# Optimization experiments

Measured on AMD Instinct MI355X. Metric: run time of the kernel, lower is better.

Reference implementation:

```python
import jax, jax.numpy as jnp
import numpy as np

B, T, P = 256, 1024, 32
HOME = 0  # home_idx from init_kwargs


def setup_inputs() -> dict:
    key = jax.random.key(0)
    k1, k2 = jax.random.split(key, 2)
    U = jax.random.normal(k1, (B, T, P), dtype=jnp.float32)
    A = jax.random.uniform(k2, (P, P), dtype=jnp.float32, minval=-0.01, maxval=0.01)
    bias = jnp.zeros((P,), dtype=jnp.float32)
    return {"unary_logits_btp": U, "A": A, "bias": bias}


def reference(unary_logits_btp, A, bias):
    """Constrained Viterbi decode (enforce at least one non-home state).
    State is (purpose p, visited-nonhome flag v in {0,1}). Returns paths (B,T) int32."""
    U = unary_logits_btp + bias  # (B,T,P), bias broadcast as in decode()
    Bn, Tn, Pn = U.shape
    NEG = jnp.finfo(U.dtype).min / 4
    is_home = jnp.arange(Pn) == HOME  # (P,)

    # t=0: v=0 only at home, v=1 only at non-home
    d0 = jnp.where(is_home, U[:, 0], NEG)
    d1 = jnp.where(is_home, NEG, U[:, 0])
    delta0 = jnp.stack([d0, d1], axis=-1)  # (B,P,2)

    def step(delta, U_t):
        # prev{v}[b, q, p] = delta[b, q, v] + A[q, p]
        prev0 = delta[:, :, 0][:, :, None] + A  # (B,P,P)
        prev1 = delta[:, :, 1][:, :, None] + A
        a0 = jnp.argmax(prev0, axis=1).astype(jnp.int32)
        v0 = jnp.max(prev0, axis=1)  # (B,P)
        a1 = jnp.argmax(prev1, axis=1).astype(jnp.int32)
        v1 = jnp.max(prev1, axis=1)
        use1 = v1 > v0  # strict >, matching torch.where(val_from1 > val_from0, ...)
        bval = jnp.where(use1, v1, v0)
        bq = jnp.where(use1, a1, a0)
        bv = use1.astype(jnp.int32)
        # next v=0 reachable only at home (from prev v=0)
        dn0 = jnp.where(is_home, v0 + U_t, NEG)
        # next v=1: home from prev v=1; non-home from best of prev v=0/v=1
        dn1 = jnp.where(is_home, v1, bval) + U_t
        p1 = jnp.where(is_home, a1, bq)
        vv1 = jnp.where(is_home, 1, bv).astype(jnp.int32)
        delta_new = jnp.stack([dn0, dn1], axis=-1)          # (B,P,2)
        psi_p = jnp.stack([a0, p1], axis=-1)                # (B,P,2) best prev purpose
        psi_v = jnp.stack([jnp.zeros_like(vv1), vv1], -1)   # (B,P,2) best prev flag
        return delta_new, (psi_p, psi_v)

    Us = jnp.swapaxes(U, 0, 1)  # (T,B,P)
    delta_T, (psi_p, psi_v) = jax.lax.scan(step, delta0, Us[1:])  # psi_*: (T-1,B,P,2)

    last_p = jnp.argmax(delta_T[:, :, 1], axis=1).astype(jnp.int32)  # (B,)
    b_idx = jnp.arange(Bn)

    def back(carry, psi):
        y, v = carry  # (B,), (B,)
        pp, pv = psi  # (B,P,2)
        py = pp[b_idx, y, v]
        nv = pv[b_idx, y, v]
        return (py, nv), py

    _, ys = jax.lax.scan(back, (last_p, jnp.ones((Bn,), jnp.int32)), (psi_p, psi_v),
                         reverse=True)  # ys: (T-1,B) with ys[t] = y[t]
    paths = jnp.concatenate([jnp.swapaxes(ys, 0, 1), last_p[:, None]], axis=1)  # (B,T)
    return paths
```

## Files before the change

### kernel.cpp

```cpp
#include <hip/hip_runtime.h>

#define T_LEN 1024
#define P_DIM 32
#define HOME_IDX 0
#define NCHUNK 32
#define CHUNK 32


__launch_bounds__(1024, 1)
__global__ void crf_viterbi_kernel(const float* __restrict__ U,
                                   const float* __restrict__ A,
                                   const float* __restrict__ bias,
                                   int* __restrict__ out)
{
    __shared__ __align__(16) float sdelta[P_DIM];
    __shared__ unsigned char spsi[(T_LEN - 1) * P_DIM];
    __shared__ unsigned char Mmap[NCHUNK * P_DIM];
    __shared__ unsigned char ent[NCHUNK];
    __shared__ int last_p_sh;

    const int tid = threadIdx.x;
    const int b   = blockIdx.x;
    int* __restrict__ outb = out + (size_t)b * T_LEN;

    if (tid < 64) {
        const int lane = tid;
        const int p    = lane & 31;
        const int h    = lane >> 5;
        const float NEG = -(3.4028234663852886e38f / 4.0f);

        float Areg[16];
#pragma unroll
        for (int j = 0; j < 16; ++j)
            Areg[j] = A[(16 * h + j) * P_DIM + p];
        const float A0p    = A[p];
        const float A00    = A[0];
        const float bias_p = bias[p];
        const float bias0  = bias[0];
        const int   q0     = h << 4;
        const bool  is_home = (p == HOME_IDX);

        const float4* __restrict__ sd4 = (const float4*)sdelta;
        const float* __restrict__ Ub = U + (size_t)b * T_LEN * P_DIM;

        const float u00 = Ub[p] + bias_p;
        float delta1  = is_home ? NEG : u00;
        float delta0h = Ub[HOME_IDX] + bias0;

        float L0 = Ub[1 * P_DIM + p];
        float L1 = Ub[2 * P_DIM + p];
        float L2 = Ub[3 * P_DIM + p];
        float L3 = Ub[4 * P_DIM + p];

        float Ut_n = L0 + bias_p;
        float u0_n = __shfl(Ut_n, 0);

        sdelta[p] = delta1;
        float4 R0 = sd4[4 * h + 0];
        float4 R1 = sd4[4 * h + 1];
        float4 R2 = sd4[4 * h + 2];
        float4 R3 = sd4[4 * h + 3];

        float cA[16], cB[16];
        float bvp = 0.f, ovvp = 0.f, bv2 = 0.f, ovv2 = 0.f;
        bool  condp = false, cond2 = false;
        int   ia2 = 0, io2 = 0;

#define STEP(t, F1, F2, CC, CP, Lc, Lr) do {                                   \
    const float Ut  = Ut_n;                                                    \
    const float u0c = u0_n;                                                    \
    CC[0]  = R0.x + Areg[0];  CC[1]  = R0.y + Areg[1];                         \
    CC[2]  = R0.z + Areg[2];  CC[3]  = R0.w + Areg[3];                         \
    CC[4]  = R1.x + Areg[4];  CC[5]  = R1.y + Areg[5];                         \
    CC[6]  = R1.z + Areg[6];  CC[7]  = R1.w + Areg[7];                         \
    CC[8]  = R2.x + Areg[8];  CC[9]  = R2.y + Areg[9];                         \
    CC[10] = R2.z + Areg[10]; CC[11] = R2.w + Areg[11];                        \
    CC[12] = R3.x + Areg[12]; CC[13] = R3.y + Areg[13];                        \
    CC[14] = R3.z + Areg[14]; CC[15] = R3.w + Areg[15];                        \
    const float g0 = fmaxf(fmaxf(CC[0],  CC[1]),  CC[2]);                      \
    const float g1 = fmaxf(fmaxf(CC[3],  CC[4]),  CC[5]);                      \
    const float g2 = fmaxf(fmaxf(CC[6],  CC[7]),  CC[8]);                      \
    const float g3 = fmaxf(fmaxf(CC[9],  CC[10]), CC[11]);                     \
    const float g4 = fmaxf(fmaxf(CC[12], CC[13]), CC[14]);                     \
    const float h0 = fmaxf(fmaxf(g0, g1), g2);                                 \
    const float h1 = fmaxf(fmaxf(g3, g4), CC[15]);                             \
    const float bv = fmaxf(h0, h1);                                            \
            \
    const float ovv = __shfl_xor(bv, 32);                                      \
    int ia1 = 0, io1 = 0;                                                      \
    if (F1) {        \
        ia1 = q0 + 15;                                                         \
        _Pragma("unroll")                                                      \
        for (int j = 14; j >= 0; --j)                                          \
            if (CP[j] == bvp) ia1 = q0 + j;                                    \
        io1 = __shfl_xor(ia1, 32);                                             \
    }                                                                          \
    if (F2) {      \
        const int amin = (ia2 < io2) ? ia2 : io2;                              \
        int a1 = (bv2 > ovv2) ? ia2 : io2;                                     \
        a1 = (bv2 == ovv2) ? amin : a1;                                        \
        spsi[(size_t)((t) - 3) * P_DIM + p] =                                  \
            (unsigned char)(cond2 ? (a1 | 32) : 0);                            \
    }                                                                          \
    const float v1 = fmaxf(bv, ovv);              \
    const float v0 = delta0h + A0p;                                            \
    const bool  use1 = (v1 > v0);                    \
    const bool  cond = use1 || is_home;                                        \
    const float sel  = cond ? v1 : v0;                                         \
    const float dn1  = sel + Ut;                                               \
    delta0h = (delta0h + A00) + u0c;                                           \
        \
    sdelta[p] = dn1;                                                           \
    R0 = sd4[4 * h + 0];                                                       \
    R1 = sd4[4 * h + 1];                                                       \
    R2 = sd4[4 * h + 2];                                                       \
    R3 = sd4[4 * h + 3];                                                       \
                                 \
    Ut_n = (Lc) + bias_p;                                                      \
    u0_n = __shfl(Ut_n, 0);                                                    \
    { int tn = (t) + 4; if (tn > T_LEN - 1) tn = T_LEN - 1;                    \
      (Lr) = Ub[(size_t)tn * P_DIM + p]; }                                     \
                                                          \
    bv2 = bvp; ovv2 = ovvp; cond2 = condp;                                     \
    ia2 = ia1; io2 = io1;                                                      \
    bvp = bv; ovvp = ovv; condp = cond;                                        \
    delta1 = dn1;                                                              \
} while (0)

        STEP(1, 0, 0, cA, cB, L1, L0);
        STEP(2, 1, 0, cB, cA, L2, L1);
        STEP(3, 1, 1, cA, cB, L3, L2);
        for (int t = 4; t <= T_LEN - 4; t += 4) {
            STEP(t + 0, 1, 1, cB, cA, L0, L3);
            STEP(t + 1, 1, 1, cA, cB, L1, L0);
            STEP(t + 2, 1, 1, cB, cA, L2, L1);
            STEP(t + 3, 1, 1, cA, cB, L3, L2);
        }
#undef STEP

        {
            const int amin = (ia2 < io2) ? ia2 : io2;
            int a1 = (bv2 > ovv2) ? ia2 : io2;
            a1 = (bv2 == ovv2) ? amin : a1;
            spsi[(size_t)(T_LEN - 3) * P_DIM + p] =
                (unsigned char)(cond2 ? (a1 | 32) : 0);
        }
        {
            int ia = q0 + 15;
#pragma unroll
            for (int j = 14; j >= 0; --j)
                if (cA[j] == bvp) ia = q0 + j;
            const int oia  = __shfl_xor(ia, 32);
            const int amin = (ia < oia) ? ia : oia;
            int a1 = (bvp > ovvp) ? ia : oia;
            a1 = (bvp == ovvp) ? amin : a1;
            spsi[(size_t)(T_LEN - 2) * P_DIM + p] =
                (unsigned char)(condp ? (a1 | 32) : 0);
        }

        float mv = delta1;
        int   mi = p;
#pragma unroll
        for (int m = 16; m >= 1; m >>= 1) {
            float ov = __shfl_xor(mv, m);
            int   oi = __shfl_xor(mi, m);
            bool take = (ov > mv) || ((ov == mv) && (oi < mi));
            mv = take ? ov : mv;
            mi = take ? oi : mi;
        }
        if (lane == 0) {
            outb[T_LEN - 1] = mi;
            last_p_sh = mi;
        }
    }

    __syncthreads();

    {
        const int c  = tid >> 5;
        const int pp = tid & 31;
        const int i_hi = min((c + 1) * CHUNK, T_LEN - 1);
        const int i_lo = c * CHUNK;
        int y = pp, v = 1;
        for (int i = i_hi - 1; i >= i_lo; --i) {
            const int bt = spsi[i * P_DIM + y];
            const int py = v ? (bt & 31) : 0;
            const int nv = v ? ((bt >> 5) & 1) : 0;
            y = py; v = nv;
        }
        Mmap[c * P_DIM + pp] = (unsigned char)(y | (v << 5));
    }
    __syncthreads();

    if (tid == 0) {
        int y = last_p_sh, v = 1;
        for (int c = NCHUNK - 1; c >= 0; --c) {
            ent[c] = (unsigned char)(y | (v << 5));
            if (v) {
                const int m = Mmap[c * P_DIM + y];
                y = m & 31;
                v = (m >> 5) & 1;
            } else {
                y = 0; v = 0;
            }
        }
    }
    __syncthreads();

    if (tid < NCHUNK) {
        const int c = tid;
        const int i_hi = min((c + 1) * CHUNK, T_LEN - 1);
        const int i_lo = c * CHUNK;
        const int e = ent[c];
        int y = e & 31;
        int v = (e >> 5) & 1;
        for (int i = i_hi - 1; i >= i_lo; --i) {
            const int bt = spsi[i * P_DIM + y];
            const int py = v ? (bt & 31) : 0;
            const int nv = v ? ((bt >> 5) & 1) : 0;
            outb[i] = py;
            y = py; v = nv;
        }
    }
}

extern "C" void kernel_launch(void* const* d_in, const int* in_sizes, int n_in,
                              void* d_out, int out_size, void* d_ws, size_t ws_size,
                              hipStream_t stream) {
    const float* U    = (const float*)d_in[0];
    const float* A    = (const float*)d_in[1];
    const float* bias = (const float*)d_in[2];
    int* out = (int*)d_out;

    const int B = in_sizes[0] / (T_LEN * P_DIM);
    crf_viterbi_kernel<<<B, 1024, 0, stream>>>(U, A, bias, out);
}
```

Before: 304.5 us.

## Remove cross-half shuffle from Viterbi critical path via split partial-max buffer

Each half-wave now writes its own partial max, combined with the v0 candidate and the unary term, into a double-width shared buffer. Every lane reads both halves' 16 entries and folds them with fmax during the next step's candidate computation. This takes the cross-half __shfl_xor and the v1/v0 select out of the serial recurrence. The use1/cond decisions needed for backpointers are recomputed later, off the critical path. In exchange each step does twice the LDS reads and extra fmax operations, and needs more registers.

```diff
diff --git a/kernel.cpp b/kernel.cpp
--- a/kernel.cpp
+++ b/kernel.cpp
@@ -13,7 +13,7 @@
                                    const float* __restrict__ bias,
                                    int* __restrict__ out)
 {
-    __shared__ __align__(16) float sdelta[P_DIM];
+    __shared__ __align__(16) float sw[2 * P_DIM];
     __shared__ unsigned char spsi[(T_LEN - 1) * P_DIM];
     __shared__ unsigned char Mmap[NCHUNK * P_DIM];
     __shared__ unsigned char ent[NCHUNK];
@@ -40,11 +40,11 @@
         const int   q0     = h << 4;
         const bool  is_home = (p == HOME_IDX);
 
-        const float4* __restrict__ sd4 = (const float4*)sdelta;
+        const float4* __restrict__ sw4 = (const float4*)sw;
         const float* __restrict__ Ub = U + (size_t)b * T_LEN * P_DIM;
 
         const float u00 = Ub[p] + bias_p;
-        float delta1  = is_home ? NEG : u00;
+        const float dinit = is_home ? NEG : u00;
         float delta0h = Ub[HOME_IDX] + bias0;
 
         float L0 = Ub[1 * P_DIM + p];
@@ -55,28 +55,39 @@
         float Ut_n = L0 + bias_p;
         float u0_n = __shfl(Ut_n, 0);
 
-        sdelta[p] = delta1;
-        float4 R0 = sd4[4 * h + 0];
-        float4 R1 = sd4[4 * h + 1];
-        float4 R2 = sd4[4 * h + 2];
-        float4 R3 = sd4[4 * h + 3];
+        sw[h * 32 + p] = h ? NEG : dinit;
+        float4 R0 = sw4[4 * h + 0], R1 = sw4[4 * h + 1];
+        float4 R2 = sw4[4 * h + 2], R3 = sw4[4 * h + 3];
+        float4 R4 = sw4[8 + 4 * h + 0], R5 = sw4[8 + 4 * h + 1];
+        float4 R6 = sw4[8 + 4 * h + 2], R7 = sw4[8 + 4 * h + 3];
 
         float cA[16], cB[16];
         float bvp = 0.f, ovvp = 0.f, bv2 = 0.f, ovv2 = 0.f;
-        bool  condp = false, cond2 = false;
+        float v0p = 0.f, v02 = 0.f;
         int   ia2 = 0, io2 = 0;
+        float w_keep = 0.f;
 
 #define STEP(t, F1, F2, CC, CP, Lc, Lr) do {                                   \
     const float Ut  = Ut_n;                                                    \
     const float u0c = u0_n;                                                    \
-    CC[0]  = R0.x + Areg[0];  CC[1]  = R0.y + Areg[1];                         \
-    CC[2]  = R0.z + Areg[2];  CC[3]  = R0.w + Areg[3];                         \
-    CC[4]  = R1.x + Areg[4];  CC[5]  = R1.y + Areg[5];                         \
-    CC[6]  = R1.z + Areg[6];  CC[7]  = R1.w + Areg[7];                         \
-    CC[8]  = R2.x + Areg[8];  CC[9]  = R2.y + Areg[9];                         \
-    CC[10] = R2.z + Areg[10]; CC[11] = R2.w + Areg[11];                        \
-    CC[12] = R3.x + Areg[12]; CC[13] = R3.y + Areg[13];                        \
-    CC[14] = R3.z + Areg[14]; CC[15] = R3.w + Areg[15];                        \
+    const float v0  = delta0h + A0p;                   \
+        \
+    CC[0]  = fmaxf(R0.x + Areg[0],  R4.x + Areg[0]);                           \
+    CC[1]  = fmaxf(R0.y + Areg[1],  R4.y + Areg[1]);                           \
+    CC[2]  = fmaxf(R0.z + Areg[2],  R4.z + Areg[2]);                           \
+    CC[3]  = fmaxf(R0.w + Areg[3],  R4.w + Areg[3]);                           \
+    CC[4]  = fmaxf(R1.x + Areg[4],  R5.x + Areg[4]);                           \
+    CC[5]  = fmaxf(R1.y + Areg[5],  R5.y + Areg[5]);                           \
+    CC[6]  = fmaxf(R1.z + Areg[6],  R5.z + Areg[6]);                           \
+    CC[7]  = fmaxf(R1.w + Areg[7],  R5.w + Areg[7]);                           \
+    CC[8]  = fmaxf(R2.x + Areg[8],  R6.x + Areg[8]);                           \
+    CC[9]  = fmaxf(R2.y + Areg[9],  R6.y + Areg[9]);                           \
+    CC[10] = fmaxf(R2.z + Areg[10], R6.z + Areg[10]);                          \
+    CC[11] = fmaxf(R2.w + Areg[11], R6.w + Areg[11]);                          \
+    CC[12] = fmaxf(R3.x + Areg[12], R7.x + Areg[12]);                          \
+    CC[13] = fmaxf(R3.y + Areg[13], R7.y + Areg[13]);                          \
+    CC[14] = fmaxf(R3.z + Areg[14], R7.z + Areg[14]);                          \
+    CC[15] = fmaxf(R3.w + Areg[15], R7.w + Areg[15]);                          \
     const float g0 = fmaxf(fmaxf(CC[0],  CC[1]),  CC[2]);                      \
     const float g1 = fmaxf(fmaxf(CC[3],  CC[4]),  CC[5]);                      \
     const float g2 = fmaxf(fmaxf(CC[6],  CC[7]),  CC[8]);                      \
@@ -85,46 +96,44 @@
     const float h0 = fmaxf(fmaxf(g0, g1), g2);                                 \
     const float h1 = fmaxf(fmaxf(g3, g4), CC[15]);                             \
     const float bv = fmaxf(h0, h1);                                            \
-            \
-    const float ovv = __shfl_xor(bv, 32);                                      \
+       \
+    const float vx = h ? NEG : (is_home ? NEG : v0);                           \
+    const float w  = fmaxf(bv, vx) + Ut;                                       \
+    delta0h = (delta0h + A00) + u0c;                                           \
+    sw[h * 32 + p] = w;                                  \
+    R0 = sw4[4 * h + 0]; R1 = sw4[4 * h + 1];             \
+    R2 = sw4[4 * h + 2]; R3 = sw4[4 * h + 3];                                  \
+    R4 = sw4[8 + 4 * h + 0]; R5 = sw4[8 + 4 * h + 1];                          \
+    R6 = sw4[8 + 4 * h + 2]; R7 = sw4[8 + 4 * h + 3];                          \
+       \
     int ia1 = 0, io1 = 0;                                                      \
-    if (F1) {        \
+    if (F1) {             \
         ia1 = q0 + 15;                                                         \
         _Pragma("unroll")                                                      \
         for (int j = 14; j >= 0; --j)                                          \
             if (CP[j] == bvp) ia1 = q0 + j;                                    \
         io1 = __shfl_xor(ia1, 32);                                             \
     }                                                                          \
+    const float ovvc = __shfl_xor(bv, 32);                                     \
     if (F2) {      \
+        const float v1_2 = fmaxf(bv2, ovv2);                                   \
+        const bool  cond2 = (v1_2 > v02) || is_home;                           \
         const int amin = (ia2 < io2) ? ia2 : io2;                              \
         int a1 = (bv2 > ovv2) ? ia2 : io2;                                     \
         a1 = (bv2 == ovv2) ? amin : a1;                                        \
         spsi[(size_t)((t) - 3) * P_DIM + p] =                                  \
             (unsigned char)(cond2 ? (a1 | 32) : 0);                            \
     }                                                                          \
-    const float v1 = fmaxf(bv, ovv);              \
-    const float v0 = delta0h + A0p;                                            \
-    const bool  use1 = (v1 > v0);                    \
-    const bool  cond = use1 || is_home;                                        \
-    const float sel  = cond ? v1 : v0;                                         \
-    const float dn1  = sel + Ut;                                               \
-    delta0h = (delta0h + A00) + u0c;                                           \
-        \
-    sdelta[p] = dn1;                                                           \
-    R0 = sd4[4 * h + 0];                                                       \
-    R1 = sd4[4 * h + 1];                                                       \
-    R2 = sd4[4 * h + 2];                                                       \
-    R3 = sd4[4 * h + 3];                                                       \
                                  \
     Ut_n = (Lc) + bias_p;                                                      \
     u0_n = __shfl(Ut_n, 0);                                                    \
     { int tn = (t) + 4; if (tn > T_LEN - 1) tn = T_LEN - 1;                    \
       (Lr) = Ub[(size_t)tn * P_DIM + p]; }                                     \
                                                           \
-    bv2 = bvp; ovv2 = ovvp; cond2 = condp;                                     \
+    bv2 = bvp; ovv2 = ovvp; v02 = v0p;                                         \
     ia2 = ia1; io2 = io1;                                                      \
-    bvp = bv; ovvp = ovv; condp = cond;                                        \
-    delta1 = dn1;                                                              \
+    bvp = bv; ovvp = ovvc; v0p = v0;                                           \
+    w_keep = w;                                                                \
 } while (0)
 
         STEP(1, 0, 0, cA, cB, L1, L0);
@@ -139,6 +148,8 @@
 #undef STEP
 
         {
+            const float v1_2 = fmaxf(bv2, ovv2);
+            const bool  cond2 = (v1_2 > v02) || is_home;
             const int amin = (ia2 < io2) ? ia2 : io2;
             int a1 = (bv2 > ovv2) ? ia2 : io2;
             a1 = (bv2 == ovv2) ? amin : a1;
@@ -151,6 +162,8 @@
             for (int j = 14; j >= 0; --j)
                 if (cA[j] == bvp) ia = q0 + j;
             const int oia  = __shfl_xor(ia, 32);
+            const float v1p = fmaxf(bvp, ovvp);
+            const bool  condp = (v1p > v0p) || is_home;
             const int amin = (ia < oia) ? ia : oia;
             int a1 = (bvp > ovvp) ? ia : oia;
             a1 = (bvp == ovvp) ? amin : a1;
@@ -158,6 +171,8 @@
                 (unsigned char)(condp ? (a1 | 32) : 0);
         }
 
+        const float ow = __shfl_xor(w_keep, 32);
+        const float delta1 = fmaxf(w_keep, ow);
         float mv = delta1;
         int   mi = p;
 #pragma unroll
```

New measurement: 346.0 us. 1.14x slower.
